# Kernel optimization log

Hardware: AMD Instinct MI355X
Metric: run time of the kernel (lower is better)

## Reference

```python
import jax, jax.numpy as jnp
import numpy as np

N = 100000   # total nodes across all graphs
E = 1600000  # directed edges
G = 2048     # number of graphs in the batch
F_IN = 10    # len(ATOM_TYPES)
LATENT = 64


def setup_inputs() -> dict:
    key = jax.random.key(0)
    ks = jax.random.split(key, 13)

    def lin_w(k, fi, fo):
        return (jax.random.normal(k, (fi, fo), dtype=jnp.float32) / np.sqrt(fi)).astype(jnp.float32)

    return {
        "x": jax.random.normal(ks[0], (N, F_IN), dtype=jnp.float32),
        "edge_index": jax.random.randint(ks[1], (2, E), 0, N),
        "batch": jnp.sort(jax.random.randint(ks[2], (N,), 0, G)),
        "W1": lin_w(ks[3], F_IN, 128), "b1": 0.01 * jax.random.normal(ks[4], (128,), dtype=jnp.float32),
        "W2": lin_w(ks[5], 128, 256), "b2": 0.01 * jax.random.normal(ks[6], (256,), dtype=jnp.float32),
        "W3": lin_w(ks[7], 256, 256), "b3": 0.01 * jax.random.normal(ks[8], (256,), dtype=jnp.float32),
        "Wmu": lin_w(ks[9], 256, LATENT), "bmu": 0.01 * jax.random.normal(ks[10], (LATENT,), dtype=jnp.float32),
        "Wlv": lin_w(ks[11], 256, LATENT), "blv": 0.01 * jax.random.normal(ks[12], (LATENT,), dtype=jnp.float32),
    }


def reference(x, edge_index, batch, W1, b1, W2, b2, W3, b3, Wmu, bmu, Wlv, blv):
    n = x.shape[0]
    # GCNConv: add self-loops, symmetric degree normalization (PyG semantics)
    loop = jnp.arange(n)
    src = jnp.concatenate([edge_index[0], loop])  # message source j
    dst = jnp.concatenate([edge_index[1], loop])  # aggregation target i
    deg = jax.ops.segment_sum(jnp.ones(src.shape[0], x.dtype), dst, num_segments=n)
    dis = jnp.where(deg > 0, jax.lax.rsqrt(jnp.maximum(deg, 1e-12)), 0.0)
    norm = (dis[src] * dis[dst])[:, None]  # [E+N, 1]

    def gcn(h, W, b):
        h = h @ W                                   # transform first (cheaper gather)
        msg = h[src] * norm                         # gather + scale
        return jax.ops.segment_sum(msg, dst, num_segments=n) + b  # scatter-add

    h = jax.nn.relu(gcn(x, W1, b1))
    h = jax.nn.relu(gcn(h, W2, b2))
    h = jax.nn.relu(gcn(h, W3, b3))

    # global_mean_pool over graph ids
    sums = jax.ops.segment_sum(h, batch, num_segments=G)               # [G, 256]
    cnt = jax.ops.segment_sum(jnp.ones((n,), h.dtype), batch, num_segments=G)
    pooled = sums / jnp.maximum(cnt, 1.0)[:, None]

    return (pooled @ Wmu + bmu, pooled @ Wlv + blv)
```

## Files before the change

kernel.cpp:

```cpp
#include <hip/hip_runtime.h>
#include <hip/hip_bf16.h>
#include <math.h>


#define THREADS 256
#define SCAN_CHUNK 4096

typedef __attribute__((ext_vector_type(8))) short bf16x8;
typedef __attribute__((ext_vector_type(4))) float f32x4;

__global__ void setup_kernel(int* deg,
                             const float* __restrict__ W2, __hip_bfloat16* __restrict__ W2T,
                             const float* __restrict__ W3, __hip_bfloat16* __restrict__ W3T,
                             const int* __restrict__ batch, int* goff,
                             int n, int g) {
    int i = blockIdx.x * blockDim.x + threadIdx.x;
    if (i < n) deg[i] = 1;
    int r2 = i - n;
    if (r2 >= 0 && r2 < 128 * 256) {
        int k = r2 >> 8, c = r2 & 255;
        W2T[c * 128 + k] = __float2bfloat16(W2[r2]);
    }
    int r3 = i - n - 128 * 256;
    if (r3 >= 0 && r3 < 256 * 256) {
        int k = r3 >> 8, c = r3 & 255;
        W3T[c * 256 + k] = __float2bfloat16(W3[r3]);
    }
    int r4 = i - n - 128 * 256 - 256 * 256;
    if (r4 >= 0 && r4 < n) {
        int j = r4;
        int b = batch[j];
        if (j == 0) {
            for (int q = 0; q <= b; ++q) goff[q] = 0;
        } else {
            int bp = batch[j - 1];
            for (int q = bp + 1; q <= b; ++q) goff[q] = j;
        }
        if (j == n - 1) {
            for (int q = b + 1; q <= g; ++q) goff[q] = n;
        }
    }
}

__global__ __launch_bounds__(THREADS) void hist_deg_kernel(
        const int* __restrict__ dst, int* deg, int e, int n) {
    const int slice = blockIdx.x & 7;
    const int sliceSize = (n + 7) / 8;
    const int lo = slice * sliceSize;
    const int hi = lo + sliceSize;
    const int tid = (blockIdx.x >> 3) * blockDim.x + threadIdx.x;
    const int nthr = (gridDim.x >> 3) * blockDim.x;
    for (int i = tid; i < e; i += nthr) {
        int d = dst[i];
        if (d >= lo && d < hi) atomicAdd(&deg[d], 1);
    }
}

__global__ __launch_bounds__(1024) void scan_part_kernel(
        const int* __restrict__ deg, int* __restrict__ bsum, int n) {
    __shared__ int ws[16];
    const int lane = threadIdx.x & 63;
    const int wid = threadIdx.x >> 6;
    int i0 = blockIdx.x * SCAN_CHUNK + threadIdx.x * 4;
    int s = 0;
#pragma unroll
    for (int q = 0; q < 4; ++q) {
        int i = i0 + q;
        if (i < n) s += deg[i] - 1;
    }
#pragma unroll
    for (int off = 32; off > 0; off >>= 1) s += __shfl_down(s, off, 64);
    if (lane == 0) ws[wid] = s;
    __syncthreads();
    if (threadIdx.x == 0) {
        int t = 0;
        for (int w = 0; w < 16; ++w) t += ws[w];
        bsum[blockIdx.x] = t;
    }
}

__global__ __launch_bounds__(1024) void scan_final_kernel(
        const int* __restrict__ deg, const int* __restrict__ bsum, int nb,
        int* __restrict__ row_ptr, int* __restrict__ cursor,
        float* __restrict__ dis, int n) {
    __shared__ int wsum[16];
    __shared__ int sbase;
    const int lane = threadIdx.x & 63;
    const int wid = threadIdx.x >> 6;
    if (threadIdx.x == 0) {
        int t = 0;
        for (int b = 0; b < blockIdx.x; ++b) t += bsum[b];
        sbase = t;
        if (blockIdx.x == 0) {
            int tot = 0;
            for (int b = 0; b < nb; ++b) tot += bsum[b];
            row_ptr[n] = tot;
        }
    }
    int i0 = blockIdx.x * SCAN_CHUNK + threadIdx.x * 4;
    int v[4];
#pragma unroll
    for (int q = 0; q < 4; ++q) {
        int i = i0 + q;
        v[q] = (i < n) ? (deg[i] - 1) : 0;
    }
    int tsum = v[0] + v[1] + v[2] + v[3];
    int incl = tsum;
#pragma unroll
    for (int off = 1; off < 64; off <<= 1) {
        int t = __shfl_up(incl, off, 64);
        if (lane >= off) incl += t;
    }
    if (lane == 63) wsum[wid] = incl;
    __syncthreads();
    int wbase = 0;
    for (int w = 0; w < wid; ++w) wbase += wsum[w];
    int pos = incl - tsum + wbase + sbase;
#pragma unroll
    for (int q = 0; q < 4; ++q) {
        int i = i0 + q;
        if (i < n) {
            row_ptr[i] = pos;
            cursor[i] = pos;
            dis[i] = rsqrtf((float)(v[q] + 1));
        }
        pos += v[q];
    }
}

__global__ __launch_bounds__(THREADS) void fill_csr_kernel(
        const int* __restrict__ src, const int* __restrict__ dst,
        int* cursor, int* __restrict__ col, int e, int n) {
    const int slice = blockIdx.x & 7;
    const int sliceSize = (n + 7) / 8;
    const int lo = slice * sliceSize;
    const int hi = lo + sliceSize;
    const int tid = (blockIdx.x >> 3) * blockDim.x + threadIdx.x;
    const int nthr = (gridDim.x >> 3) * blockDim.x;
    for (int i = tid; i < e; i += nthr) {
        int d = dst[i];
        if (d >= lo && d < hi) {
            int pos = atomicAdd(&cursor[d], 1);
            col[pos] = src[i];
        }
    }
}

__device__ __forceinline__ void acc8(float* acc, uint4 v) {
    acc[0] += __uint_as_float(v.x << 16);
    acc[1] += __uint_as_float(v.x & 0xffff0000u);
    acc[2] += __uint_as_float(v.y << 16);
    acc[3] += __uint_as_float(v.y & 0xffff0000u);
    acc[4] += __uint_as_float(v.z << 16);
    acc[5] += __uint_as_float(v.z & 0xffff0000u);
    acc[6] += __uint_as_float(v.w << 16);
    acc[7] += __uint_as_float(v.w & 0xffff0000u);
}

__device__ __forceinline__ unsigned pack2(float a, float b) {
    unsigned short ua = __builtin_bit_cast(unsigned short, __float2bfloat16(a));
    unsigned short ub = __builtin_bit_cast(unsigned short, __float2bfloat16(b));
    return (unsigned)ua | ((unsigned)ub << 16);
}

__global__ __launch_bounds__(THREADS) void layer1_kernel(
        const float* __restrict__ x, const int* __restrict__ row_ptr,
        const int* __restrict__ col, const float* __restrict__ dis,
        const float* __restrict__ W1, const float* __restrict__ b1,
        __hip_bfloat16* __restrict__ out, int n) {
    __shared__ float h[16][12];
    __shared__ float w[10][128];
    __shared__ float bias[128];

    for (int idx = threadIdx.x; idx < 1280; idx += THREADS)
        w[idx >> 7][idx & 127] = W1[idx];
    if (threadIdx.x < 128) bias[threadIdx.x] = b1[threadIdx.x];

    const int node0 = blockIdx.x * 16;
    const int sub = threadIdx.x >> 4;
    const int lane = threadIdx.x & 15;
    const int node = node0 + sub;
    const bool act = (lane < 10) && (node < n);

    float acc = 0.f;
    float dn = 1.f;
    if (act) {
        dn = dis[node];
        acc = x[(size_t)node * 10 + lane] * dn;
        int s = row_ptr[node], e = row_ptr[node + 1];
        int p = s;
        for (; p + 8 <= e; p += 8) {
            int j[8];
#pragma unroll
            for (int q = 0; q < 8; ++q) j[q] = col[p + q];
            float v[8];
#pragma unroll
            for (int q = 0; q < 8; ++q) v[q] = x[(size_t)j[q] * 10 + lane] * dis[j[q]];
#pragma unroll
            for (int q = 0; q < 8; ++q) acc += v[q];
        }
        for (; p < e; ++p) {
            int j = col[p];
            acc += x[(size_t)j * 10 + lane] * dis[j];
        }
        acc *= dn;
    }
    if (lane < 12) h[sub][lane] = (lane < 10) ? acc : 0.f;
    __syncthreads();

    const int r = threadIdx.x >> 4;
    const int c0 = (threadIdx.x & 15) * 8;
    const int nodeB = node0 + r;
    if (nodeB < n) {
        float dnB = dis[nodeB];
        float hv[10];
#pragma unroll
        for (int k = 0; k < 10; ++k) hv[k] = h[r][k];
        uint4 res;
        unsigned rr[4];
#pragma unroll
        for (int cc = 0; cc < 8; cc += 2) {
            float a0 = bias[c0 + cc], a1 = bias[c0 + cc + 1];
#pragma unroll
            for (int k = 0; k < 10; ++k) {
                a0 = fmaf(hv[k], w[k][c0 + cc], a0);
                a1 = fmaf(hv[k], w[k][c0 + cc + 1], a1);
            }
            rr[cc >> 1] = pack2(fmaxf(a0, 0.f) * dnB, fmaxf(a1, 0.f) * dnB);
        }
        res.x = rr[0]; res.y = rr[1]; res.z = rr[2]; res.w = rr[3];
        reinterpret_cast<uint4*>(out)[((size_t)nodeB * 128 + c0) >> 3] = res;
    }
}

template <int COLS, int L>
__global__ __launch_bounds__(THREADS) void agg_bf16_kernel(
        const __hip_bfloat16* __restrict__ S, const int* __restrict__ row_ptr,
        const int* __restrict__ col, const float* __restrict__ dis,
        __hip_bfloat16* __restrict__ out, int n) {
    static_assert(L * 8 == COLS, "");
    constexpr int stride = COLS / 8;
    int node = blockIdx.x * (THREADS / L) + threadIdx.x / L;
    if (node >= n) return;
    int lane = threadIdx.x % L;
    const uint4* S4 = reinterpret_cast<const uint4*>(S);

    float acc[8];
#pragma unroll
    for (int q = 0; q < 8; ++q) acc[q] = 0.f;
    acc8(acc, S4[(size_t)node * stride + lane]);

    int s = row_ptr[node], e = row_ptr[node + 1];
    int p = s;
    for (; p + 8 <= e; p += 8) {
        int j[8];
#pragma unroll
        for (int q = 0; q < 8; ++q) j[q] = col[p + q];
        uint4 v[8];
#pragma unroll
        for (int q = 0; q < 8; ++q) v[q] = S4[(size_t)j[q] * stride + lane];
#pragma unroll
        for (int q = 0; q < 8; ++q) acc8(acc, v[q]);
    }
    for (; p + 2 <= e; p += 2) {
        int j0 = col[p], j1 = col[p + 1];
        uint4 v0 = S4[(size_t)j0 * stride + lane];
        uint4 v1 = S4[(size_t)j1 * stride + lane];
        acc8(acc, v0); acc8(acc, v1);
    }
    for (; p < e; ++p) acc8(acc, S4[(size_t)col[p] * stride + lane]);

    float d = dis[node];
    uint4 o;
    o.x = pack2(acc[0] * d, acc[1] * d);
    o.y = pack2(acc[2] * d, acc[3] * d);
    o.z = pack2(acc[4] * d, acc[5] * d);
    o.w = pack2(acc[6] * d, acc[7] * d);
    reinterpret_cast<uint4*>(out)[(size_t)node * stride + lane] = o;
}

template <int K, bool SCALE>
__global__ __launch_bounds__(THREADS) void transform_mfma2_kernel(
        const __hip_bfloat16* __restrict__ A, const __hip_bfloat16* __restrict__ WT,
        const float* __restrict__ b, const float* __restrict__ dis,
        __hip_bfloat16* __restrict__ out, int n, int ntiles) {
    constexpr int KS = K / 32;
    const int wave = threadIdx.x >> 6;
    const int lane = threadIdx.x & 63;
    const int lrow = lane & 15;
    const int lk8  = (lane >> 4) * 8;

    const uint4* WT4 = reinterpret_cast<const uint4*>(WT);
    bf16x8 bfr[4][KS];
    float bias[4];
#pragma unroll
    for (int ct = 0; ct < 4; ++ct) {
        int colc = wave * 64 + ct * 16 + lrow;
        bias[ct] = b[colc];
#pragma unroll
        for (int kk = 0; kk < KS; ++kk)
            bfr[ct][kk] = __builtin_bit_cast(
                bf16x8, WT4[((size_t)colc * K + kk * 32 + lk8) >> 3]);
    }

    const uint4* A4 = reinterpret_cast<const uint4*>(A);
    auto loadA = [&](int t, uint4* av) {
        int row = t * 16 + lrow;
        if (row >= n) row = n - 1;
#pragma unroll
        for (int kk = 0; kk < KS; ++kk)
            av[kk] = A4[((size_t)row * K + kk * 32 + lk8) >> 3];
    };

    uint4 aC[KS], aN[KS];
    int t = blockIdx.x;
    if (t < ntiles) loadA(t, aC);

    for (; t < ntiles; t += gridDim.x) {
        int tn = t + gridDim.x;
        if (tn < ntiles) loadA(tn, aN);

        f32x4 acc[4];
#pragma unroll
        for (int ct = 0; ct < 4; ++ct) acc[ct] = (f32x4){0.f, 0.f, 0.f, 0.f};
#pragma unroll
        for (int kk = 0; kk < KS; ++kk) {
            bf16x8 af = __builtin_bit_cast(bf16x8, aC[kk]);
#pragma unroll
            for (int ct = 0; ct < 4; ++ct)
                acc[ct] = __builtin_amdgcn_mfma_f32_16x16x32_bf16(af, bfr[ct][kk], acc[ct], 0, 0, 0);
        }

        const int orow0 = t * 16 + (lane >> 4) * 4;
        float dv[4];
#pragma unroll
        for (int r = 0; r < 4; ++r) {
            int rr = orow0 + r;
            dv[r] = SCALE ? ((rr < n) ? dis[rr] : 0.f) : 1.f;
        }
#pragma unroll
        for (int ct = 0; ct < 4; ++ct) {
            int colc = wave * 64 + ct * 16 + lrow;
#pragma unroll
            for (int r = 0; r < 4; ++r) {
                int rr = orow0 + r;
                if (rr < n) {
                    float v = fmaxf(acc[ct][r] + bias[ct], 0.f);
                    if (SCALE) v *= dv[r];
                    out[(size_t)rr * 256 + colc] = __float2bfloat16(v);
                }
            }
        }
#pragma unroll
        for (int kk = 0; kk < KS; ++kk) aC[kk] = aN[kk];
    }
}

__global__ __launch_bounds__(THREADS) void pool_heads_kernel(
        const __hip_bfloat16* __restrict__ H, const int* __restrict__ goff,
        const float* __restrict__ Wmu, const float* __restrict__ bmu,
        const float* __restrict__ Wlv, const float* __restrict__ blv,
        float* __restrict__ out, int g_total) {
    __shared__ float p[256];
    int g = blockIdx.x;
    int c = threadIdx.x;
    int s = goff[g], e = goff[g + 1];
    float acc = 0.f;
    for (int r = s; r < e; ++r) acc += __bfloat162float(H[(size_t)r * 256 + c]);
    p[c] = acc / fmaxf((float)(e - s), 1.0f);
    __syncthreads();
    if (threadIdx.x < 128) {
        int cc = threadIdx.x & 63;
        bool is_mu = threadIdx.x < 64;
        const float* W = is_mu ? Wmu : Wlv;
        const float* bb = is_mu ? bmu : blv;
        float a = 0.f;
        for (int k = 0; k < 256; ++k) a = fmaf(p[k], W[k * 64 + cc], a);
        float* o = is_mu ? (out + (size_t)g * 64)
                         : (out + (size_t)g_total * 64 + (size_t)g * 64);
        o[cc] = a + bb[cc];
    }
}

extern "C" void kernel_launch(void* const* d_in, const int* in_sizes, int n_in,
                              void* d_out, int out_size, void* d_ws, size_t ws_size,
                              hipStream_t stream) {
    const float* x      = (const float*)d_in[0];
    const int*   eidx   = (const int*)d_in[1];
    const int*   batch  = (const int*)d_in[2];
    const float* W1  = (const float*)d_in[3];
    const float* b1  = (const float*)d_in[4];
    const float* W2  = (const float*)d_in[5];
    const float* b2  = (const float*)d_in[6];
    const float* W3  = (const float*)d_in[7];
    const float* b3  = (const float*)d_in[8];
    const float* Wmu = (const float*)d_in[9];
    const float* bmu = (const float*)d_in[10];
    const float* Wlv = (const float*)d_in[11];
    const float* blv = (const float*)d_in[12];
    float* out = (float*)d_out;

    const int N = in_sizes[0] / 10;
    const int E = in_sizes[1] / 2;
    const int G = out_size / 128;

    const int* src = eidx;
    const int* dst = eidx + E;

    __hip_bfloat16* SA = (__hip_bfloat16*)d_ws;
    __hip_bfloat16* SB = SA + (size_t)N * 256;
    float* dis  = (float*)(SB + (size_t)N * 256);
    __hip_bfloat16* W2T = (__hip_bfloat16*)(dis + N);
    __hip_bfloat16* W3T = W2T + 256 * 128;
    int* deg     = (int*)(W3T + 256 * 256);
    int* row_ptr = deg + N;
    int* cursor  = row_ptr + N + 1;
    int* col     = cursor + N;
    int* goff    = col + E;
    int* bsum    = goff + G + 1;

    const int ntiles = (N + 15) / 16;
    const int nb = (N + SCAN_CHUNK - 1) / SCAN_CHUNK;

    {
        int total = 2 * N + 128 * 256 + 256 * 256;
        setup_kernel<<<(total + THREADS - 1) / THREADS, THREADS, 0, stream>>>(
            deg, W2, W2T, W3, W3T, batch, goff, N, G);
    }
    hist_deg_kernel<<<2048, THREADS, 0, stream>>>(dst, deg, E, N);
    scan_part_kernel<<<nb, 1024, 0, stream>>>(deg, bsum, N);
    scan_final_kernel<<<nb, 1024, 0, stream>>>(deg, bsum, nb, row_ptr, cursor, dis, N);
    fill_csr_kernel<<<2048, THREADS, 0, stream>>>(src, dst, cursor, col, E, N);

    layer1_kernel<<<(N + 15) / 16, THREADS, 0, stream>>>(
        x, row_ptr, col, dis, W1, b1, SA, N);

    agg_bf16_kernel<128, 16><<<(N + 15) / 16, THREADS, 0, stream>>>(SA, row_ptr, col, dis, SB, N);
    transform_mfma2_kernel<128, true><<<512, THREADS, 0, stream>>>(SB, W2T, b2, dis, SA, N, ntiles);

    agg_bf16_kernel<256, 32><<<(N + 7) / 8, THREADS, 0, stream>>>(SA, row_ptr, col, dis, SB, N);
    transform_mfma2_kernel<256, false><<<512, THREADS, 0, stream>>>(SB, W3T, b3, dis, SA, N, ntiles);

    pool_heads_kernel<<<G, THREADS, 0, stream>>>(SA, goff, Wmu, bmu, Wlv, blv, out, G);
}
```

Baseline: 484.2 us.

## Vectorize edge loads, prescale x into padded bf16 rows, widen layer1 and pooling

Histogram and CSR fill now read dst and src as uint4, four edges per load. The fill kernel skips the src load when none of the four destinations fall in its slice. The scan kernel also writes a dis-prescaled, 16-wide padded bf16 copy of x, so layer1 gathers one 16-byte half-row per neighbour instead of ten scattered floats plus a dis lookup. Layer1 now uses 2 threads per node and 128 nodes per block, and pooling reads rows with vectorized loads split across 8 row groups. The cost is an extra workspace buffer and bf16 rounding of the layer-1 inputs.

```diff
diff --git a/kernel.cpp b/kernel.cpp
--- a/kernel.cpp
+++ b/kernel.cpp
@@ -50,7 +50,16 @@
     const int hi = lo + sliceSize;
     const int tid = (blockIdx.x >> 3) * blockDim.x + threadIdx.x;
     const int nthr = (gridDim.x >> 3) * blockDim.x;
-    for (int i = tid; i < e; i += nthr) {
+    const int e4 = e >> 2;
+    const uint4* dst4 = reinterpret_cast<const uint4*>(dst);
+    for (int i = tid; i < e4; i += nthr) {
+        uint4 dv = dst4[i];
+        int dd[4] = {(int)dv.x, (int)dv.y, (int)dv.z, (int)dv.w};
+#pragma unroll
+        for (int q = 0; q < 4; ++q)
+            if (dd[q] >= lo && dd[q] < hi) atomicAdd(&deg[dd[q]], 1);
+    }
+    for (int i = (e & ~3) + tid; i < e; i += nthr) {
         int d = dst[i];
         if (d >= lo && d < hi) atomicAdd(&deg[d], 1);
     }
@@ -79,10 +88,17 @@
     }
 }
 
+__device__ __forceinline__ unsigned pack2(float a, float b) {
+    unsigned short ua = __builtin_bit_cast(unsigned short, __float2bfloat16(a));
+    unsigned short ub = __builtin_bit_cast(unsigned short, __float2bfloat16(b));
+    return (unsigned)ua | ((unsigned)ub << 16);
+}
+
 __global__ __launch_bounds__(1024) void scan_final_kernel(
         const int* __restrict__ deg, const int* __restrict__ bsum, int nb,
         int* __restrict__ row_ptr, int* __restrict__ cursor,
-        float* __restrict__ dis, int n) {
+        float* __restrict__ dis, const float* __restrict__ x,
+        __hip_bfloat16* __restrict__ xd, int n) {
     __shared__ int wsum[16];
     __shared__ int sbase;
     const int lane = threadIdx.x & 63;
@@ -116,13 +132,23 @@
     int wbase = 0;
     for (int w = 0; w < wid; ++w) wbase += wsum[w];
     int pos = incl - tsum + wbase + sbase;
+    uint4* xd4 = reinterpret_cast<uint4*>(xd);
 #pragma unroll
     for (int q = 0; q < 4; ++q) {
         int i = i0 + q;
         if (i < n) {
             row_ptr[i] = pos;
             cursor[i] = pos;
-            dis[i] = rsqrtf((float)(v[q] + 1));
+            float dv = rsqrtf((float)(v[q] + 1));
+            dis[i] = dv;
+            unsigned ow[8];
+#pragma unroll
+            for (int k = 0; k < 5; ++k)
+                ow[k] = pack2(x[(size_t)i * 10 + 2 * k] * dv,
+                              x[(size_t)i * 10 + 2 * k + 1] * dv);
+            ow[5] = 0; ow[6] = 0; ow[7] = 0;
+            xd4[(size_t)i * 2]     = make_uint4(ow[0], ow[1], ow[2], ow[3]);
+            xd4[(size_t)i * 2 + 1] = make_uint4(ow[4], ow[5], ow[6], ow[7]);
         }
         pos += v[q];
     }
@@ -137,7 +163,27 @@
     const int hi = lo + sliceSize;
     const int tid = (blockIdx.x >> 3) * blockDim.x + threadIdx.x;
     const int nthr = (gridDim.x >> 3) * blockDim.x;
-    for (int i = tid; i < e; i += nthr) {
+    const int e4 = e >> 2;
+    const uint4* dst4 = reinterpret_cast<const uint4*>(dst);
+    const uint4* src4 = reinterpret_cast<const uint4*>(src);
+    for (int i = tid; i < e4; i += nthr) {
+        uint4 dv = dst4[i];
+        int dd[4] = {(int)dv.x, (int)dv.y, (int)dv.z, (int)dv.w};
+        bool any = false;
+#pragma unroll
+        for (int q = 0; q < 4; ++q) any |= (dd[q] >= lo && dd[q] < hi);
+        if (!any) continue;
+        uint4 sv = src4[i];
+        int ss[4] = {(int)sv.x, (int)sv.y, (int)sv.z, (int)sv.w};
+#pragma unroll
+        for (int q = 0; q < 4; ++q) {
+            if (dd[q] >= lo && dd[q] < hi) {
+                int pos = atomicAdd(&cursor[dd[q]], 1);
+                col[pos] = ss[q];
+            }
+        }
+    }
+    for (int i = (e & ~3) + tid; i < e; i += nthr) {
         int d = dst[i];
         if (d >= lo && d < hi) {
             int pos = atomicAdd(&cursor[d], 1);
@@ -157,18 +203,12 @@
     acc[7] += __uint_as_float(v.w & 0xffff0000u);
 }
 
-__device__ __forceinline__ unsigned pack2(float a, float b) {
-    unsigned short ua = __builtin_bit_cast(unsigned short, __float2bfloat16(a));
-    unsigned short ub = __builtin_bit_cast(unsigned short, __float2bfloat16(b));
-    return (unsigned)ua | ((unsigned)ub << 16);
-}
-
 __global__ __launch_bounds__(THREADS) void layer1_kernel(
-        const float* __restrict__ x, const int* __restrict__ row_ptr,
+        const __hip_bfloat16* __restrict__ xd, const int* __restrict__ row_ptr,
         const int* __restrict__ col, const float* __restrict__ dis,
         const float* __restrict__ W1, const float* __restrict__ b1,
         __hip_bfloat16* __restrict__ out, int n) {
-    __shared__ float h[16][12];
+    __shared__ float h[128][12];
     __shared__ float w[10][128];
     __shared__ float bias[128];
 
@@ -176,60 +216,67 @@
         w[idx >> 7][idx & 127] = W1[idx];
     if (threadIdx.x < 128) bias[threadIdx.x] = b1[threadIdx.x];
 
-    const int node0 = blockIdx.x * 16;
-    const int sub = threadIdx.x >> 4;
-    const int lane = threadIdx.x & 15;
-    const int node = node0 + sub;
-    const bool act = (lane < 10) && (node < n);
-
-    float acc = 0.f;
-    float dn = 1.f;
-    if (act) {
-        dn = dis[node];
-        acc = x[(size_t)node * 10 + lane] * dn;
+    const int node0 = blockIdx.x * 128;
+    const int nl = threadIdx.x >> 1;
+    const int lane = threadIdx.x & 1;
+    const int node = node0 + nl;
+    const uint4* S4 = reinterpret_cast<const uint4*>(xd);
+
+    if (node < n) {
+        float acc[8];
+#pragma unroll
+        for (int q = 0; q < 8; ++q) acc[q] = 0.f;
+        acc8(acc, S4[(size_t)node * 2 + lane]);
+
         int s = row_ptr[node], e = row_ptr[node + 1];
         int p = s;
         for (; p + 8 <= e; p += 8) {
             int j[8];
 #pragma unroll
             for (int q = 0; q < 8; ++q) j[q] = col[p + q];
-            float v[8];
-#pragma unroll
-            for (int q = 0; q < 8; ++q) v[q] = x[(size_t)j[q] * 10 + lane] * dis[j[q]];
-#pragma unroll
-            for (int q = 0; q < 8; ++q) acc += v[q];
-        }
-        for (; p < e; ++p) {
-            int j = col[p];
-            acc += x[(size_t)j * 10 + lane] * dis[j];
-        }
-        acc *= dn;
-    }
-    if (lane < 12) h[sub][lane] = (lane < 10) ? acc : 0.f;
+            uint4 v[8];
+#pragma unroll
+            for (int q = 0; q < 8; ++q) v[q] = S4[(size_t)j[q] * 2 + lane];
+#pragma unroll
+            for (int q = 0; q < 8; ++q) acc8(acc, v[q]);
+        }
+        for (; p < e; ++p) acc8(acc, S4[(size_t)col[p] * 2 + lane]);
+
+        float dn = dis[node];
+        if (lane == 0) {
+#pragma unroll
+            for (int q = 0; q < 8; ++q) h[nl][q] = acc[q] * dn;
+        } else {
+            h[nl][8] = acc[0] * dn;
+            h[nl][9] = acc[1] * dn;
+        }
+    }
     __syncthreads();
 
-    const int r = threadIdx.x >> 4;
-    const int c0 = (threadIdx.x & 15) * 8;
-    const int nodeB = node0 + r;
+    const int half = threadIdx.x & 1;
+    const int nodeB = node0 + (threadIdx.x >> 1);
     if (nodeB < n) {
         float dnB = dis[nodeB];
         float hv[10];
 #pragma unroll
-        for (int k = 0; k < 10; ++k) hv[k] = h[r][k];
-        uint4 res;
-        unsigned rr[4];
-#pragma unroll
-        for (int cc = 0; cc < 8; cc += 2) {
-            float a0 = bias[c0 + cc], a1 = bias[c0 + cc + 1];
-#pragma unroll
-            for (int k = 0; k < 10; ++k) {
-                a0 = fmaf(hv[k], w[k][c0 + cc], a0);
-                a1 = fmaf(hv[k], w[k][c0 + cc + 1], a1);
+        for (int k = 0; k < 10; ++k) hv[k] = h[threadIdx.x >> 1][k];
+#pragma unroll
+        for (int step = 0; step < 8; ++step) {
+            int c0 = half * 64 + step * 8;
+            unsigned rr[4];
+#pragma unroll
+            for (int cc = 0; cc < 8; cc += 2) {
+                float a0 = bias[c0 + cc], a1 = bias[c0 + cc + 1];
+#pragma unroll
+                for (int k = 0; k < 10; ++k) {
+                    a0 = fmaf(hv[k], w[k][c0 + cc], a0);
+                    a1 = fmaf(hv[k], w[k][c0 + cc + 1], a1);
+                }
+                rr[cc >> 1] = pack2(fmaxf(a0, 0.f) * dnB, fmaxf(a1, 0.f) * dnB);
             }
-            rr[cc >> 1] = pack2(fmaxf(a0, 0.f) * dnB, fmaxf(a1, 0.f) * dnB);
-        }
-        res.x = rr[0]; res.y = rr[1]; res.z = rr[2]; res.w = rr[3];
-        reinterpret_cast<uint4*>(out)[((size_t)nodeB * 128 + c0) >> 3] = res;
+            reinterpret_cast<uint4*>(out)[((size_t)nodeB * 128 + c0) >> 3] =
+                make_uint4(rr[0], rr[1], rr[2], rr[3]);
+        }
     }
 }
 
@@ -361,14 +408,30 @@
         const float* __restrict__ Wmu, const float* __restrict__ bmu,
         const float* __restrict__ Wlv, const float* __restrict__ blv,
         float* __restrict__ out, int g_total) {
+    __shared__ float part[8][256];
     __shared__ float p[256];
     int g = blockIdx.x;
+    int s = goff[g], e = goff[g + 1];
+    int rgrp = threadIdx.x >> 5;
+    int lane = threadIdx.x & 31;
+    const uint4* H4 = reinterpret_cast<const uint4*>(H);
+
+    float acc[8];
+#pragma unroll
+    for (int q = 0; q < 8; ++q) acc[q] = 0.f;
+    for (int r = s + rgrp; r < e; r += 8)
+        acc8(acc, H4[(size_t)r * 32 + lane]);
+#pragma unroll
+    for (int q = 0; q < 8; ++q) part[rgrp][lane * 8 + q] = acc[q];
+    __syncthreads();
+
     int c = threadIdx.x;
-    int s = goff[g], e = goff[g + 1];
-    float acc = 0.f;
-    for (int r = s; r < e; ++r) acc += __bfloat162float(H[(size_t)r * 256 + c]);
-    p[c] = acc / fmaxf((float)(e - s), 1.0f);
+    float t = 0.f;
+#pragma unroll
+    for (int gq = 0; gq < 8; ++gq) t += part[gq][c];
+    p[c] = t / fmaxf((float)(e - s), 1.0f);
     __syncthreads();
+
     if (threadIdx.x < 128) {
         int cc = threadIdx.x & 63;
         bool is_mu = threadIdx.x < 64;
@@ -412,7 +475,8 @@
     float* dis  = (float*)(SB + (size_t)N * 256);
     __hip_bfloat16* W2T = (__hip_bfloat16*)(dis + N);
     __hip_bfloat16* W3T = W2T + 256 * 128;
-    int* deg     = (int*)(W3T + 256 * 256);
+    __hip_bfloat16* xd  = W3T + 256 * 256;
+    int* deg     = (int*)(xd + (size_t)N * 16);
     int* row_ptr = deg + N;
     int* cursor  = row_ptr + N + 1;
     int* col     = cursor + N;
@@ -429,11 +493,11 @@
     }
     hist_deg_kernel<<<2048, THREADS, 0, stream>>>(dst, deg, E, N);
     scan_part_kernel<<<nb, 1024, 0, stream>>>(deg, bsum, N);
-    scan_final_kernel<<<nb, 1024, 0, stream>>>(deg, bsum, nb, row_ptr, cursor, dis, N);
+    scan_final_kernel<<<nb, 1024, 0, stream>>>(deg, bsum, nb, row_ptr, cursor, dis, x, xd, N);
     fill_csr_kernel<<<2048, THREADS, 0, stream>>>(src, dst, cursor, col, E, N);
 
-    layer1_kernel<<<(N + 15) / 16, THREADS, 0, stream>>>(
-        x, row_ptr, col, dis, W1, b1, SA, N);
+    layer1_kernel<<<(N + 127) / 128, THREADS, 0, stream>>>(
+        xd, row_ptr, col, dis, W1, b1, SA, N);
 
     agg_bf16_kernel<128, 16><<<(N + 15) / 16, THREADS, 0, stream>>>(SA, row_ptr, col, dis, SB, N);
     transform_mfma2_kernel<128, true><<<512, THREADS, 0, stream>>>(SB, W2T, b2, dis, SA, N, ntiles);
```

Measured after the change: 477.7 us. No clear change (-1.3%).
